# Kernel optimization log

Hardware: AMD Instinct MI355X
Metric: run time of the kernel (lower is better)

Reference implementation:

```python
import jax, jax.numpy as jnp
import numpy as np

K = 8
HID = 32
BOUND = 5.0
SIGMA_MIN = 1e-4
MIN_DERIV = 1e-3
B, T, C = 32, 4096, 512


def setup_inputs() -> dict:
    key = jax.random.key(0)
    k1, k2, k3 = jax.random.split(key, 3)
    x = jax.random.normal(k1, (B, T, C), jnp.float32)
    W1 = jax.random.normal(k2, (HID, 2), jnp.float32) * 0.5
    b1 = jnp.zeros((HID,), jnp.float32)
    W2 = jax.random.normal(k3, (3 * K + 1, HID), jnp.float32) * 0.1
    b2 = jnp.zeros((3 * K + 1,), jnp.float32)
    return {"x": x, "W1": W1, "b1": b1, "W2": W2, "b2": b2}


def _rqs_forward(x2d, kx, ky, d):
    # x2d: (BC, T); kx, ky, d: (BC, K+1)
    w = kx[:, 1:] - kx[:, :-1]
    h = ky[:, 1:] - ky[:, :-1]
    s = h / jnp.maximum(w, 1e-8)
    idx = jax.vmap(lambda a, v: jnp.searchsorted(a, v, side='right'))(kx, x2d) - 1
    idx = jnp.clip(idx, 0, K - 1)  # (BC, T)
    g = lambda t, i: jnp.take_along_axis(t, i, axis=1)
    w_k = g(w, idx)
    h_k = g(h, idx)
    s_k = g(s, idx)
    d_k = g(d, idx)
    d_k1 = g(d, jnp.minimum(idx + 1, K))
    kx_l = g(kx, idx)
    ky_l = g(ky, idx)
    zeta = jnp.clip((x2d - kx_l) / jnp.maximum(w_k, 1e-8), 0.0, 1.0)
    numer = h_k * (s_k * zeta * zeta + d_k * zeta * (1.0 - zeta))
    denom = s_k + (d_k1 + d_k - 2.0 * s_k) * zeta * (1.0 - zeta)
    z2d = ky_l + numer / jnp.maximum(denom, 1e-8)
    tail = (x2d < -BOUND) | (x2d > BOUND)
    return jnp.where(tail, x2d, z2d)


def reference(x, W1, b1, W2, b2):
    Bb, Tt, Cc = x.shape
    # affine standardisation (unbiased std matching torch.std default)
    mu = jnp.mean(x, axis=1, keepdims=True)
    sig = jnp.maximum(jnp.std(x, axis=1, ddof=1, keepdims=True), SIGMA_MIN)
    z_pre = (x - mu) / sig  # (B, T, C)
    zd = jax.lax.stop_gradient(z_pre)
    skew = jnp.mean(zd ** 3, axis=1)          # (B, C)
    ekurt = jnp.mean(zd ** 4, axis=1) - 3.0   # (B, C)
    stats = jnp.stack([skew, ekurt], axis=-1).reshape(Bb * Cc, 2)
    hid = jax.nn.relu(stats @ W1.T + b1)
    raw = hid @ W2.T + b2                      # (BC, 3K+1)
    widths = jax.nn.softmax(raw[:, :K], axis=-1) * (2.0 * BOUND)
    heights = jax.nn.softmax(raw[:, K:2 * K], axis=-1) * (2.0 * BOUND)
    derivs = jax.nn.softplus(raw[:, 2 * K:]) + MIN_DERIV  # (BC, K+1)
    pad = jnp.full((widths.shape[0], 1), -BOUND, widths.dtype)
    kx = jnp.concatenate([pad, -BOUND + jnp.cumsum(widths, axis=-1)], axis=-1)
    ky = jnp.concatenate([pad, -BOUND + jnp.cumsum(heights, axis=-1)], axis=-1)
    x2d = jnp.transpose(z_pre, (0, 2, 1)).reshape(Bb * Cc, Tt)
    z2d = _rqs_forward(x2d, kx, ky, derivs)
    return jnp.transpose(z2d.reshape(Bb, Cc, Tt), (0, 2, 1))
```

## Files before the change

### kernel.cpp

```cpp
#include <hip/hip_runtime.h>
#include <math.h>

#define KNOTS 8
#define HIDN 32
#define TT 4096
#define CC 512
#define NB 32
#define BOUNDF 5.0f
#define CT 32
#define NTG 32
#define TPT (TT / NTG)

__global__ __launch_bounds__(1024, 8)
void k_fused(const float* __restrict__ x, const float* __restrict__ W1,
             const float* __restrict__ b1, const float* __restrict__ W2,
             const float* __restrict__ b2, float* __restrict__ out)
{
    const int bb = blockIdx.y;
    const int c0 = blockIdx.x * CT;
    const int ci = threadIdx.x & (CT - 1);
    const int tg = threadIdx.x >> 5;

    __shared__ float red[NTG][4][CT];
    __shared__ float mom[4][CT];
    __shared__ float pA[CT], pB[CT];
    __shared__ float pKx[7][CT];
    __shared__ float4 binsA[KNOTS][CT];
    __shared__ float4 binsB[KNOTS][CT];

    const size_t base = (size_t)bb * TT * CC + c0 + ci;
    const float* pxt = x + base + (size_t)tg * CC;

    float s1 = 0.f, s2 = 0.f, s3 = 0.f, s4 = 0.f;
    #pragma unroll 8
    for (int k = 0; k < TPT; ++k) {
        float v  = pxt[(size_t)k * (NTG * CC)];
        float v2 = v * v;
        s1 += v;
        s2 = fmaf(v,  v,  s2);
        s3 = fmaf(v2, v,  s3);
        s4 = fmaf(v2, v2, s4);
    }
    red[tg][0][ci] = s1; red[tg][1][ci] = s2;
    red[tg][2][ci] = s3; red[tg][3][ci] = s4;
    __syncthreads();

    if (threadIdx.x < 4 * CT) {
        const int m = threadIdx.x >> 5, c = threadIdx.x & (CT - 1);
        float acc = 0.f;
        #pragma unroll
        for (int g = 0; g < NTG; ++g) acc += red[g][m][c];
        mom[m][c] = acc;
    }
    __syncthreads();

    if (threadIdx.x < CT) {
        const int c = threadIdx.x;
        const float n  = (float)TT;
        const float t1 = mom[0][c], t2 = mom[1][c], t3 = mom[2][c], t4 = mom[3][c];
        const float mu  = t1 / n;
        const float ex2 = t2 / n, ex3 = t3 / n, ex4 = t4 / n;
        float var = (t2 - n * mu * mu) / (n - 1.f);
        var = fmaxf(var, 0.f);
        const float sig  = fmaxf(sqrtf(var), 1e-4f);
        const float inv  = 1.f / sig;
        const float mu2  = mu * mu;
        const float ez3  = ex3 - 3.f * mu * ex2 + 2.f * mu * mu2;
        const float ez4  = ex4 - 4.f * mu * ex3 + 6.f * mu2 * ex2 - 3.f * mu2 * mu2;
        const float inv2 = inv * inv;
        const float skew  = ez3 * inv2 * inv;
        const float ekurt = ez4 * inv2 * inv2 - 3.f;

        float hid[HIDN];
        #pragma unroll
        for (int h = 0; h < HIDN; ++h) {
            float v = fmaf(W1[2*h], skew, fmaf(W1[2*h+1], ekurt, b1[h]));
            hid[h] = fmaxf(v, 0.f);
        }

        float e[KNOTS], kxr[KNOTS+1], kyr[KNOTS+1], dr[KNOTS+1];
        {
            float mx = -1e30f;
            #pragma unroll
            for (int o = 0; o < KNOTS; ++o) {
                float acc = b2[o];
                #pragma unroll
                for (int h = 0; h < HIDN; ++h) acc = fmaf(W2[o*HIDN + h], hid[h], acc);
                e[o] = acc; mx = fmaxf(mx, acc);
            }
            float sum = 0.f;
            #pragma unroll
            for (int o = 0; o < KNOTS; ++o) { e[o] = expf(e[o] - mx); sum += e[o]; }
            const float scale = (2.f * BOUNDF) / sum;
            float cum = -BOUNDF; kxr[0] = -BOUNDF;
            #pragma unroll
            for (int o = 0; o < KNOTS; ++o) { cum = fmaf(e[o], scale, cum); kxr[o+1] = cum; }
        }
        {
            float mx = -1e30f;
            #pragma unroll
            for (int o = 0; o < KNOTS; ++o) {
                float acc = b2[KNOTS + o];
                #pragma unroll
                for (int h = 0; h < HIDN; ++h) acc = fmaf(W2[(KNOTS+o)*HIDN + h], hid[h], acc);
                e[o] = acc; mx = fmaxf(mx, acc);
            }
            float sum = 0.f;
            #pragma unroll
            for (int o = 0; o < KNOTS; ++o) { e[o] = expf(e[o] - mx); sum += e[o]; }
            const float scale = (2.f * BOUNDF) / sum;
            float cum = -BOUNDF; kyr[0] = -BOUNDF;
            #pragma unroll
            for (int o = 0; o < KNOTS; ++o) { cum = fmaf(e[o], scale, cum); kyr[o+1] = cum; }
        }
        #pragma unroll
        for (int o = 0; o < KNOTS+1; ++o) {
            float acc = b2[2*KNOTS + o];
            #pragma unroll
            for (int h = 0; h < HIDN; ++h) acc = fmaf(W2[(2*KNOTS+o)*HIDN + h], hid[h], acc);
            float sp = fmaxf(acc, 0.f) + log1pf(expf(-fabsf(acc)));
            dr[o] = sp + 1e-3f;
        }

        pA[c] = inv;
        pB[c] = -mu * inv;
        #pragma unroll
        for (int j = 1; j <= 7; ++j) pKx[j-1][c] = kxr[j];
        #pragma unroll
        for (int j = 0; j < KNOTS; ++j) {
            const float w  = kxr[j+1] - kxr[j];
            const float wm = fmaxf(w, 1e-8f);
            const float h  = kyr[j+1] - kyr[j];
            const float s  = h / wm;
            float4 A, Bq;
            A.x = kxr[j];  A.y = 1.f / wm;  A.z = kyr[j];  A.w = h * s;
            Bq.x = h * dr[j];  Bq.y = dr[j+1] + dr[j] - 2.f * s;  Bq.z = s;  Bq.w = 0.f;
            binsA[j][c] = A;
            binsB[j][c] = Bq;
        }
    }
    __syncthreads();

    const float a  = pA[ci];
    const float bz = pB[ci];
    const float kx1 = pKx[0][ci], kx2 = pKx[1][ci], kx3 = pKx[2][ci],
                kx4 = pKx[3][ci], kx5 = pKx[4][ci], kx6 = pKx[5][ci],
                kx7 = pKx[6][ci];
    float* pot = out + base + (size_t)tg * CC;

    for (int kb = TPT / 8 - 1; kb >= 0; --kb) {
        float xv[8];
        #pragma unroll
        for (int j = 0; j < 8; ++j)
            xv[j] = pxt[(size_t)(kb * 8 + j) * (NTG * CC)];
        #pragma unroll
        for (int j = 0; j < 8; ++j) {
            const float z = fmaf(xv[j], a, bz);
            const int idx = (z >= kx1) + (z >= kx2) + (z >= kx3) + (z >= kx4)
                          + (z >= kx5) + (z >= kx6) + (z >= kx7);
            const float4 A  = binsA[idx][ci];
            const float4 Bq = binsB[idx][ci];
            float zeta = (z - A.x) * A.y;
            zeta = fminf(fmaxf(zeta, 0.f), 1.f);
            const float u     = zeta - zeta * zeta;
            const float numer = fmaf(A.w * zeta, zeta, Bq.x * u);
            const float denom = fmaf(Bq.y, u, Bq.z);
            const float res   = fmaf(numer, __builtin_amdgcn_rcpf(fmaxf(denom, 1e-8f)), A.z);
            const float o = (fabsf(z) > BOUNDF) ? z : res;
            __builtin_nontemporal_store(o, &pot[(size_t)(kb * 8 + j) * (NTG * CC)]);
        }
    }
}

extern "C" void kernel_launch(void* const* d_in, const int* in_sizes, int n_in,
                              void* d_out, int out_size, void* d_ws, size_t ws_size,
                              hipStream_t stream) {
    const float* x  = (const float*)d_in[0];
    const float* W1 = (const float*)d_in[1];
    const float* b1 = (const float*)d_in[2];
    const float* W2 = (const float*)d_in[3];
    const float* b2 = (const float*)d_in[4];
    float* out = (float*)d_out;

    k_fused<<<dim3(CC / CT, NB), dim3(1024), 0, stream>>>(x, W1, b1, W2, b2, out);
}
```

Baseline: 146.3 us.

## Pack spline bin params into one float4 with fp16, branchless binary search, halve block

Block size drops from 1024 to 512 threads (NTG 16), so each thread handles twice as many time steps. Per-bin parameters are now packed into a single float4, with knot y, height and derivatives stored as fp16 pairs, which halves the shared-memory loads per element. The linear 7-compare bin search becomes a 3-level select-based binary search, and zeta is computed with one FMA using a precomputed offset. The zeta clamp is dropped and the fp16 storage lowers parameter precision, which risks accuracy loss against the fp32 reference.

```diff
diff --git a/kernel.cpp b/kernel.cpp
--- a/kernel.cpp
+++ b/kernel.cpp
@@ -8,10 +8,13 @@
 #define NB 32
 #define BOUNDF 5.0f
 #define CT 32
-#define NTG 32
+#define NTG 16
 #define TPT (TT / NTG)
 
-__global__ __launch_bounds__(1024, 8)
+typedef _Float16 f16x2 __attribute__((ext_vector_type(2)));
+union F32H { float f; f16x2 h; };
+
+__global__ __launch_bounds__(512, 4)
 void k_fused(const float* __restrict__ x, const float* __restrict__ W1,
              const float* __restrict__ b1, const float* __restrict__ W2,
              const float* __restrict__ b2, float* __restrict__ out)
@@ -25,8 +28,7 @@
     __shared__ float mom[4][CT];
     __shared__ float pA[CT], pB[CT];
     __shared__ float pKx[7][CT];
-    __shared__ float4 binsA[KNOTS][CT];
-    __shared__ float4 binsB[KNOTS][CT];
+    __shared__ float4 bins[KNOTS * CT];
 
     const size_t base = (size_t)bb * TT * CC + c0 + ci;
     const float* pxt = x + base + (size_t)tg * CC;
@@ -128,15 +130,17 @@
         for (int j = 1; j <= 7; ++j) pKx[j-1][c] = kxr[j];
         #pragma unroll
         for (int j = 0; j < KNOTS; ++j) {
-            const float w  = kxr[j+1] - kxr[j];
-            const float wm = fmaxf(w, 1e-8f);
-            const float h  = kyr[j+1] - kyr[j];
-            const float s  = h / wm;
-            float4 A, Bq;
-            A.x = kxr[j];  A.y = 1.f / wm;  A.z = kyr[j];  A.w = h * s;
-            Bq.x = h * dr[j];  Bq.y = dr[j+1] + dr[j] - 2.f * s;  Bq.z = s;  Bq.w = 0.f;
-            binsA[j][c] = A;
-            binsB[j][c] = Bq;
+            const float w    = kxr[j+1] - kxr[j];
+            const float wm   = fmaxf(w, 1e-8f);
+            const float invw = 1.f / wm;
+            const float h    = kyr[j+1] - kyr[j];
+            float4 A;
+            A.x = -kxr[j] * invw;
+            A.y = invw;
+            F32H p; p.h.x = (_Float16)kyr[j]; p.h.y = (_Float16)h;
+            F32H q; q.h.x = (_Float16)dr[j];  q.h.y = (_Float16)(dr[j] + dr[j+1]);
+            A.z = p.f;  A.w = q.f;
+            bins[j * CT + c] = A;
         }
     }
     __syncthreads();
@@ -156,16 +160,30 @@
         #pragma unroll
         for (int j = 0; j < 8; ++j) {
             const float z = fmaf(xv[j], a, bz);
-            const int idx = (z >= kx1) + (z >= kx2) + (z >= kx3) + (z >= kx4)
-                          + (z >= kx5) + (z >= kx6) + (z >= kx7);
-            const float4 A  = binsA[idx][ci];
-            const float4 Bq = binsB[idx][ci];
-            float zeta = (z - A.x) * A.y;
-            zeta = fminf(fmaxf(zeta, 0.f), 1.f);
-            const float u     = zeta - zeta * zeta;
-            const float numer = fmaf(A.w * zeta, zeta, Bq.x * u);
-            const float denom = fmaf(Bq.y, u, Bq.z);
-            const float res   = fmaf(numer, __builtin_amdgcn_rcpf(fmaxf(denom, 1e-8f)), A.z);
+            const bool  c4 = z >= kx4;
+            const float mB = c4 ? kx6 : kx2;
+            const bool  cB = z >= mB;
+            const float nLo = c4 ? kx5 : kx1;
+            const float nHi = c4 ? kx7 : kx3;
+            const float mC = cB ? nHi : nLo;
+            const bool  cC = z >= mC;
+            const int off = (c4 ? 4*CT : 0) + (cB ? 2*CT : 0) + (cC ? CT : 0) + ci;
+            const float4 A = bins[off];
+
+            const float zeta = fmaf(z, A.y, A.x);
+            const float u    = fmaf(-zeta, zeta, zeta);
+            F32H p; p.f = A.z;
+            F32H q; q.f = A.w;
+            const float kyl = (float)p.h.x;
+            const float h   = (float)p.h.y;
+            const float d0  = (float)q.h.x;
+            const float D01 = (float)q.h.y;
+            const float s   = h * A.y;
+            const float R   = fmaf(-2.f, s, D01);
+            const float den = fmaf(R, u, s);
+            const float inner = fmaf(s * zeta, zeta, d0 * u);
+            const float res = fmaf(h * inner,
+                                   __builtin_amdgcn_rcpf(fmaxf(den, 1e-8f)), kyl);
             const float o = (fabsf(z) > BOUNDF) ? z : res;
             __builtin_nontemporal_store(o, &pot[(size_t)(kb * 8 + j) * (NTG * CC)]);
         }
@@ -182,5 +200,5 @@
     const float* b2 = (const float*)d_in[4];
     float* out = (float*)d_out;
 
-    k_fused<<<dim3(CC / CT, NB), dim3(1024), 0, stream>>>(x, W1, b1, W2, b2, out);
+    k_fused<<<dim3(CC / CT, NB), dim3(512), 0, stream>>>(x, W1, b1, W2, b2, out);
 }
```

New measurement: 129.1 us. -11.7%, faster.
